# Kernel tuning notes

Measured on AMD Instinct MI355X. Metric: run time of the kernel, lower is better.

## Reference

```python
import jax, jax.numpy as jnp
import numpy as np

B, S, K, N = 4, 2048, 4096, 16384

def setup_inputs() -> dict:
    key = jax.random.key(0)
    k1, k2, k3, k4 = jax.random.split(key, 4)
    x = jax.random.normal(k1, (B, S, K), dtype=jnp.float32)
    weight_data = jax.random.randint(k2, (N, K), -127, 128, dtype=jnp.int32)  # holds int8-range values
    scale = jax.random.uniform(k3, (N, 1), dtype=jnp.float32, minval=0.001, maxval=0.02)
    bias = jax.random.normal(k4, (N,), dtype=jnp.float32)
    return {"x": x, "weight_data": weight_data, "scale": scale, "bias": bias}

def reference(x, weight_data, scale, bias):
    x_shape = x.shape
    x_flat = x.reshape(-1, K)                      # [M, K]
    max_val = jnp.max(jnp.abs(x_flat), axis=1, keepdims=True)  # [M, 1]
    scale_x = max_val / 127.0
    scale_x = jnp.where(scale_x == 0, jnp.float32(1.0), scale_x)
    x_int8 = jnp.clip(jnp.round(x_flat / scale_x), -127, 127).astype(jnp.int8)
    w_int8 = weight_data.astype(jnp.int8)          # [N, K]
    # int8 GEMM with int32 accumulation (torch._int_mm equivalent)
    y_int32 = jax.lax.dot_general(
        x_int8, w_int8.T,
        dimension_numbers=(((1,), (0,)), ((), ())),
        preferred_element_type=jnp.int32)           # [M, N]
    y = y_int32.astype(jnp.float32) * scale_x * scale.reshape(1, -1)
    y = y.reshape(x_shape[0], x_shape[1], N)
    y = y + bias
    return y
```

## Files before the change

### kernel.cpp

```cpp
#include <hip/hip_runtime.h>
#include <hip/hip_bf16.h>
#include <cstdint>

#define MDIM 8192
#define KDIM 4096
#define NDIM 16384

typedef int v4i __attribute__((ext_vector_type(4)));

__device__ __forceinline__ void gload_lds16(const void* g, void* l) {
    __builtin_amdgcn_global_load_lds(
        (const __attribute__((address_space(1))) int*)g,
        (__attribute__((address_space(3))) int*)l, 16, 0, 0);
}

__global__ __launch_bounds__(256) void conv_w(const int4* __restrict__ w,
                                              int* __restrict__ wq) {
    int g = blockIdx.x * 256 + threadIdx.x;
    int4 v = w[g];
    unsigned p = (unsigned)(v.x & 255) | ((unsigned)(v.y & 255) << 8) |
                 ((unsigned)(v.z & 255) << 16) | ((unsigned)(v.w & 255) << 24);
    wq[g] = (int)p;
}

__global__ __launch_bounds__(256) void quant_rows(const float* __restrict__ x,
                                                  int* __restrict__ xq32,
                                                  float* __restrict__ sx) {
    const int row = blockIdx.x;
    const int t = threadIdx.x;
    const float4* xr = (const float4*)(x + (size_t)row * KDIM);

    float4 v[4];
    float amax = 0.f;
#pragma unroll
    for (int p = 0; p < 4; ++p) {
        v[p] = xr[p * 256 + t];
        amax = fmaxf(amax, fmaxf(fmaxf(fabsf(v[p].x), fabsf(v[p].y)),
                                 fmaxf(fabsf(v[p].z), fabsf(v[p].w))));
    }
#pragma unroll
    for (int off = 32; off > 0; off >>= 1)
        amax = fmaxf(amax, __shfl_down(amax, off));
    __shared__ float wmax[4];
    int wave = t >> 6, lane = t & 63;
    if (lane == 0) wmax[wave] = amax;
    __syncthreads();
    float m = fmaxf(fmaxf(wmax[0], wmax[1]), fmaxf(wmax[2], wmax[3]));

    float inv = (m > 0.f) ? 127.f / m : 0.f;
    if (t == 0) {
        float s = m / 127.f;
        sx[row] = (s == 0.f) ? 1.f : s;
    }

    int* out = xq32 + (size_t)row * (KDIM / 4);
#pragma unroll
    for (int p = 0; p < 4; ++p) {
        int q0 = (int)rintf(v[p].x * inv); q0 = max(-127, min(127, q0));
        int q1 = (int)rintf(v[p].y * inv); q1 = max(-127, min(127, q1));
        int q2 = (int)rintf(v[p].z * inv); q2 = max(-127, min(127, q2));
        int q3 = (int)rintf(v[p].w * inv); q3 = max(-127, min(127, q3));
        unsigned pk = (unsigned)(q0 & 255) | ((unsigned)(q1 & 255) << 8) |
                      ((unsigned)(q2 & 255) << 16) | ((unsigned)(q3 & 255) << 24);
        out[p * 256 + t] = (int)pk;
    }
}

__global__ __launch_bounds__(256) void gemm_i8(const signed char* __restrict__ xq,
                                               const signed char* __restrict__ wq,
                                               const float* __restrict__ sx,
                                               const float* __restrict__ scale,
                                               const float* __restrict__ bias,
                                               float* __restrict__ y) {
    __shared__ __align__(16) signed char lds_a[128 * 64];
    __shared__ __align__(16) signed char lds_b[128 * 64];

    const int tid = threadIdx.x;
    const int wave = tid >> 6, lane = tid & 63;
    const int quad = lane >> 4, l16 = lane & 15;
    const int tileM = blockIdx.y * 128, tileN = blockIdx.x * 128;
    const int wm = (wave >> 1) * 64, wn = (wave & 1) * 64;

    const signed char* ga = xq + (size_t)tileM * KDIM;
    const signed char* gb = wq + (size_t)tileN * KDIM;

    v4i acc[4][4] = {};

    for (int k0 = 0; k0 < KDIM; k0 += 64) {
        __syncthreads();
#pragma unroll
        for (int p = 0; p < 2; ++p) {
            int off = (p * 4 + wave) * 1024 + lane * 16;
            int mr = off >> 6;
            int kb = off & 63;
            gload_lds16(ga + (size_t)mr * KDIM + k0 + kb, lds_a + off);
            gload_lds16(gb + (size_t)mr * KDIM + k0 + kb, lds_b + off);
        }
        __syncthreads();

        v4i af[4], bf[4];
#pragma unroll
        for (int i = 0; i < 4; ++i) {
            af[i] = *(const v4i*)(lds_a + (wm + i * 16 + l16) * 64 + quad * 16);
            bf[i] = *(const v4i*)(lds_b + (wn + i * 16 + l16) * 64 + quad * 16);
        }
#pragma unroll
        for (int i = 0; i < 4; ++i)
#pragma unroll
            for (int j = 0; j < 4; ++j)
                acc[i][j] = __builtin_amdgcn_mfma_i32_16x16x64_i8(af[i], bf[j],
                                                                  acc[i][j], 0, 0, 0);
    }

#pragma unroll
    for (int j = 0; j < 4; ++j) {
        int n = tileN + wn + j * 16 + l16;
        float scn = scale[n];
        float bsn = bias[n];
#pragma unroll
        for (int i = 0; i < 4; ++i) {
#pragma unroll
            for (int r = 0; r < 4; ++r) {
                int m = tileM + wm + i * 16 + quad * 4 + r;
                y[(size_t)m * NDIM + n] =
                    (float)acc[i][j][r] * sx[m] * scn + bsn;
            }
        }
    }
}

extern "C" void kernel_launch(void* const* d_in, const int* in_sizes, int n_in,
                              void* d_out, int out_size, void* d_ws, size_t ws_size,
                              hipStream_t stream) {
    const float* x      = (const float*)d_in[0];
    const int*   wdat   = (const int*)d_in[1];
    const float* scale  = (const float*)d_in[2];
    const float* bias   = (const float*)d_in[3];
    float* y = (float*)d_out;

    signed char* wq = (signed char*)d_ws;
    signed char* xq = wq + (size_t)NDIM * KDIM;
    float*       sx = (float*)(xq + (size_t)MDIM * KDIM);

    conv_w<<<(NDIM * (size_t)KDIM) / 4 / 256, 256, 0, stream>>>((const int4*)wdat,
                                                                (int*)wq);
    quant_rows<<<MDIM, 256, 0, stream>>>(x, (int*)xq, sx);

    dim3 grid(NDIM / 128, MDIM / 128);
    gemm_i8<<<grid, 256, 0, stream>>>(xq, wq, sx, scale, bias, y);
}
```

Baseline: 1.545 ms.

## Rewrite int8 GEMM with 256x256 tiles, 4-stage LDS pipeline and swizzle

The GEMM kernel moves to 256x256 block tiles with 8 waves and a 4-deep LDS ring buffer. Global-to-LDS loads are issued three K-steps ahead, with manual waitcnt and barrier scheduling so they overlap the MFMA work. It also adds an XOR swizzle to avoid LDS bank conflicts, remaps block IDs across XCDs for L2 locality, and raises MFMA wave priority. The cost is heavier register and LDS use (128KB LDS per block while asking for 2 blocks per CU). The hand-placed vmcnt counts are fragile if the load count per stage ever changes.

```diff
diff --git a/kernel.cpp b/kernel.cpp
--- a/kernel.cpp
+++ b/kernel.cpp
@@ -1,10 +1,15 @@
 #include <hip/hip_runtime.h>
-#include <hip/hip_bf16.h>
 #include <cstdint>
 
 #define MDIM 8192
 #define KDIM 4096
 #define NDIM 16384
+
+#define BM 256
+#define BN 256
+#define BKB 64
+#define NT (KDIM / BKB)
+#define NBUF 4
 
 typedef int v4i __attribute__((ext_vector_type(4)));
 
@@ -66,67 +71,120 @@
     }
 }
 
-__global__ __launch_bounds__(256) void gemm_i8(const signed char* __restrict__ xq,
-                                               const signed char* __restrict__ wq,
-                                               const float* __restrict__ sx,
-                                               const float* __restrict__ scale,
-                                               const float* __restrict__ bias,
-                                               float* __restrict__ y) {
-    __shared__ __align__(16) signed char lds_a[128 * 64];
-    __shared__ __align__(16) signed char lds_b[128 * 64];
-
-    const int tid = threadIdx.x;
-    const int wave = tid >> 6, lane = tid & 63;
-    const int quad = lane >> 4, l16 = lane & 15;
-    const int tileM = blockIdx.y * 128, tileN = blockIdx.x * 128;
-    const int wm = (wave >> 1) * 64, wn = (wave & 1) * 64;
-
-    const signed char* ga = xq + (size_t)tileM * KDIM;
-    const signed char* gb = wq + (size_t)tileN * KDIM;
-
-    v4i acc[4][4] = {};
-
-    for (int k0 = 0; k0 < KDIM; k0 += 64) {
-        __syncthreads();
-#pragma unroll
-        for (int p = 0; p < 2; ++p) {
-            int off = (p * 4 + wave) * 1024 + lane * 16;
-            int mr = off >> 6;
-            int kb = off & 63;
-            gload_lds16(ga + (size_t)mr * KDIM + k0 + kb, lds_a + off);
-            gload_lds16(gb + (size_t)mr * KDIM + k0 + kb, lds_b + off);
-        }
-        __syncthreads();
-
-        v4i af[4], bf[4];
-#pragma unroll
-        for (int i = 0; i < 4; ++i) {
-            af[i] = *(const v4i*)(lds_a + (wm + i * 16 + l16) * 64 + quad * 16);
-            bf[i] = *(const v4i*)(lds_b + (wn + i * 16 + l16) * 64 + quad * 16);
-        }
+__global__ __launch_bounds__(512, 2) void gemm_i8(const signed char* __restrict__ xq,
+                                                  const signed char* __restrict__ wq,
+                                                  const float* __restrict__ sx,
+                                                  const float* __restrict__ scale,
+                                                  const float* __restrict__ bias,
+                                                  float* __restrict__ y) {
+    __shared__ __align__(16) signed char lds_a[NBUF][BM * BKB];
+    __shared__ __align__(16) signed char lds_b[NBUF][BN * BKB];
+
+    const int tid  = threadIdx.x;
+    const int lane = tid & 63;
+    const int wave = tid >> 6;
+    const int l16  = lane & 15;
+    const int quad = lane >> 4;
+    const int wm   = wave >> 2;
+    const int wn   = wave & 3;
+
+    int lin = blockIdx.y * gridDim.x + blockIdx.x;
+    lin = (lin & 7) * ((MDIM / BM) * (NDIM / BN) / 8) + (lin >> 3);
+    const int tileN = (lin & (NDIM / BN - 1)) * BN;
+    const int tileM = (lin >> 6) * BM;
+
+    const int srow = tid >> 2;
+    const int scol = ((tid & 3) << 4) ^ (((srow >> 1) & 3) << 4);
+    const signed char* gA0 = xq + (size_t)(tileM + srow) * KDIM + scol;
+    const signed char* gA1 = gA0 + (size_t)128 * KDIM;
+    const signed char* gB0 = wq + (size_t)(tileN + srow) * KDIM + scol;
+    const signed char* gB1 = gB0 + (size_t)128 * KDIM;
+    const int lo = tid << 4;
+
+#define STAGE_A(t) do { const int _b = (t) & (NBUF - 1);                     \
+        gload_lds16(gA0 + (size_t)(t) * BKB, &lds_a[_b][lo]);                \
+        gload_lds16(gA1 + (size_t)(t) * BKB, &lds_a[_b][lo + 8192]); } while (0)
+#define STAGE_B(t) do { const int _b = (t) & (NBUF - 1);                     \
+        gload_lds16(gB0 + (size_t)(t) * BKB, &lds_b[_b][lo]);                \
+        gload_lds16(gB1 + (size_t)(t) * BKB, &lds_b[_b][lo + 8192]); } while (0)
+
+    const int rcol = (quad << 4) ^ (((l16 >> 1) & 3) << 4);
+    const int aoff = (wm * 128 + l16) * BKB + rcol;
+    const int boff = (wn * 64 + l16) * BKB + rcol;
+
+    v4i acc[8][4] = {};
+
+    STAGE_A(0); STAGE_B(0);
+    STAGE_A(1); STAGE_B(1);
+    STAGE_A(2); STAGE_B(2);
+    asm volatile("s_waitcnt vmcnt(8)" ::: "memory");
+    __builtin_amdgcn_s_barrier();
+
+    for (int t = 0; t < NT; ++t) {
+        const signed char* la = &lds_a[t & (NBUF - 1)][0];
+        const signed char* lb = &lds_b[t & (NBUF - 1)][0];
+        v4i af[4], bf[4], ag[4];
+
+#pragma unroll
+        for (int i = 0; i < 4; ++i) af[i] = *(const v4i*)(la + aoff + i * 1024);
+#pragma unroll
+        for (int j = 0; j < 4; ++j) bf[j] = *(const v4i*)(lb + boff + j * 1024);
+        if (t + 3 < NT) STAGE_A(t + 3);
+        __builtin_amdgcn_s_barrier();
+        asm volatile("s_waitcnt lgkmcnt(0)" ::: "memory");
+        __builtin_amdgcn_sched_barrier(0);
+        __builtin_amdgcn_s_setprio(1);
 #pragma unroll
         for (int i = 0; i < 4; ++i)
 #pragma unroll
             for (int j = 0; j < 4; ++j)
                 acc[i][j] = __builtin_amdgcn_mfma_i32_16x16x64_i8(af[i], bf[j],
                                                                   acc[i][j], 0, 0, 0);
-    }
+        __builtin_amdgcn_s_setprio(0);
+        __builtin_amdgcn_s_barrier();
+
+#pragma unroll
+        for (int i = 0; i < 4; ++i) ag[i] = *(const v4i*)(la + aoff + (4 + i) * 1024);
+        if (t + 3 < NT) STAGE_B(t + 3);
+        __builtin_amdgcn_s_barrier();
+        asm volatile("s_waitcnt lgkmcnt(0)" ::: "memory");
+        __builtin_amdgcn_sched_barrier(0);
+        __builtin_amdgcn_s_setprio(1);
+#pragma unroll
+        for (int i = 0; i < 4; ++i)
+#pragma unroll
+            for (int j = 0; j < 4; ++j)
+                acc[4 + i][j] = __builtin_amdgcn_mfma_i32_16x16x64_i8(ag[i], bf[j],
+                                                                      acc[4 + i][j], 0, 0, 0);
+        __builtin_amdgcn_s_setprio(0);
+        if (t <= NT - 4)      { asm volatile("s_waitcnt vmcnt(8)" ::: "memory"); }
+        else if (t == NT - 3) { asm volatile("s_waitcnt vmcnt(4)" ::: "memory"); }
+        else if (t == NT - 2) { asm volatile("s_waitcnt vmcnt(0)" ::: "memory"); }
+        __builtin_amdgcn_s_barrier();
+    }
+
+    float sxv[8][4];
+#pragma unroll
+    for (int i = 0; i < 8; ++i)
+#pragma unroll
+        for (int r = 0; r < 4; ++r)
+            sxv[i][r] = sx[tileM + wm * 128 + i * 16 + quad * 4 + r];
 
 #pragma unroll
     for (int j = 0; j < 4; ++j) {
-        int n = tileN + wn + j * 16 + l16;
-        float scn = scale[n];
-        float bsn = bias[n];
-#pragma unroll
-        for (int i = 0; i < 4; ++i) {
-#pragma unroll
-            for (int r = 0; r < 4; ++r) {
-                int m = tileM + wm + i * 16 + quad * 4 + r;
-                y[(size_t)m * NDIM + n] =
-                    (float)acc[i][j][r] * sx[m] * scn + bsn;
-            }
+        const int n = tileN + wn * 64 + j * 16 + l16;
+        const float scn = scale[n];
+        const float bsn = bias[n];
+#pragma unroll
+        for (int i = 0; i < 8; ++i) {
+            const size_t mrow = (size_t)(tileM + wm * 128 + i * 16 + quad * 4);
+#pragma unroll
+            for (int r = 0; r < 4; ++r)
+                y[(mrow + r) * NDIM + n] = (float)acc[i][j][r] * sxv[i][r] * scn + bsn;
         }
     }
+#undef STAGE_A
+#undef STAGE_B
 }
 
 extern "C" void kernel_launch(void* const* d_in, const int* in_sizes, int n_in,
@@ -146,6 +204,6 @@
                                                                 (int*)wq);
     quant_rows<<<MDIM, 256, 0, stream>>>(x, (int*)xq, sx);
 
-    dim3 grid(NDIM / 128, MDIM / 128);
-    gemm_i8<<<grid, 256, 0, stream>>>(xq, wq, sx, scale, bias, y);
-}
+    dim3 grid(NDIM / BN, MDIM / BM);
+    gemm_i8<<<grid, 512, 0, stream>>>(xq, wq, sx, scale, bias, y);
+}
```

After: 1.376 ms. 1.12x faster.
